# Performance work log

Hardware: AMD Instinct MI355X
Metric: run time of the kernel (lower is better)

## Reference

```python
import jax, jax.numpy as jnp
import numpy as np

N_NODES = 50000
N_EDGES = 800000
D_IN = 256
D_HID = 128
NUM_LAYERS = 6
ALPHA = 0.1
THETA = 0.5
EPS = 1e-5  # BatchNorm1d default eps


def setup_inputs() -> dict:
    key = jax.random.key(0)
    ks = jax.random.split(key, 6)
    x = jax.random.normal(ks[0], (N_NODES, D_IN), dtype=jnp.float32)
    edge_index = jax.random.randint(ks[1], (2, N_EDGES), 0, N_NODES)
    # GCNConv(D_IN, D_HID): weight + bias
    W_lin = jax.random.normal(ks[2], (D_IN, D_HID), dtype=jnp.float32) / np.sqrt(D_IN).astype(np.float32)
    b_lin = jnp.zeros((D_HID,), jnp.float32)
    # GCN2Conv weight1 per layer (shared_weights=True -> only weight1, no bias)
    W1s = jax.random.normal(ks[3], (NUM_LAYERS - 1, D_HID, D_HID), dtype=jnp.float32) / np.sqrt(D_HID).astype(np.float32)
    # BatchNorm1d affine params per intermediate layer
    bn_gamma = jnp.ones((NUM_LAYERS - 2, D_HID), jnp.float32)
    bn_beta = jnp.zeros((NUM_LAYERS - 2, D_HID), jnp.float32)
    return {"x": x, "edge_index": edge_index, "W_lin": W_lin, "b_lin": b_lin,
            "W1s": W1s, "bn_gamma": bn_gamma, "bn_beta": bn_beta}


def _gcn_conv(x, W, b, edge_index):
    # PyG GCNConv: transform, add self-loops, D^{-1/2}(A+I)D^{-1/2} aggregation.
    n = x.shape[0]
    xw = x @ W  # [N, D_HID]
    loop = jnp.arange(n)
    src = jnp.concatenate([edge_index[0], loop])
    dst = jnp.concatenate([edge_index[1], loop])
    deg = jax.ops.segment_sum(jnp.ones(src.shape, xw.dtype), dst, num_segments=n)
    dinv = jax.lax.rsqrt(jnp.maximum(deg, 1.0))  # deg >= 1 thanks to self loops
    w = dinv[src] * dinv[dst]  # [E+N]
    return jax.ops.segment_sum(xw[src] * w[:, None], dst, num_segments=n) + b


def _gcn2_conv(z, x0, W1, edge_index, beta):
    # GCN2Conv with normalize=False, shared_weights=True:
    # h = (1-alpha)*sum_{j->i} z_j + alpha*x0 ; out = (1-beta)*h + beta*(h @ W1)
    n = z.shape[0]
    agg = jax.ops.segment_sum(z[edge_index[0]], edge_index[1], num_segments=n)
    h = (1.0 - ALPHA) * agg + ALPHA * x0
    return (1.0 - beta) * h + beta * (h @ W1)


def _batchnorm(z, gamma, beta_p):
    # training-mode BatchNorm1d over the node dimension (biased variance)
    mu = jnp.mean(z, axis=0)
    var = jnp.var(z, axis=0)
    return (z - mu) * jax.lax.rsqrt(var + EPS) * gamma + beta_p


def reference(x, edge_index, W_lin, b_lin, W1s, bn_gamma, bn_beta):
    z = _gcn_conv(x, W_lin, b_lin, edge_index)
    x0 = z
    n_convs = NUM_LAYERS - 1
    # GCN2Conv layer index l = i+1 -> beta_l = log(theta/l + 1)
    betas = [float(np.log(THETA / (i + 1) + 1.0)) for i in range(n_convs)]
    for i in range(n_convs):  # dropout=0.0 -> identity, omitted
        z = _gcn2_conv(z, x0, W1s[i], edge_index, betas[i])
        if i < n_convs - 1:
            z = _batchnorm(z, bn_gamma[i], bn_beta[i])
            z = jax.nn.relu(z)
    return z
```

## Files before the change

kernel.cpp:

```cpp
#include <hip/hip_runtime.h>
#include <math.h>

#define N_NODES 50000
#define N_EDGES 800000
#define D_IN 256
#define D_HID 128
#define ALPHA 0.1f
#define EPS 1e-5f

#define NBUCK 391
#define EPB 4096
#define NBLK 196

typedef __attribute__((ext_vector_type(8))) short bf16x8;
typedef __attribute__((ext_vector_type(4))) float f32x4;

static __device__ __forceinline__ unsigned short f2bf(float f) {
    unsigned int x = __float_as_uint(f);
    return (unsigned short)((x + 0x7fffu + ((x >> 16) & 1u)) >> 16);
}
static __device__ __forceinline__ float blo(unsigned int v) {
    return __uint_as_float(v << 16);
}
static __device__ __forceinline__ float bhi(unsigned int v) {
    return __uint_as_float(v & 0xffff0000u);
}

__global__ __launch_bounds__(256) void k_hist(const int* __restrict__ dst,
                                              int* __restrict__ hist, int e) {
    __shared__ int h[NBUCK];
    int t = threadIdx.x;
    for (int i = t; i < NBUCK; i += 256) h[i] = 0;
    __syncthreads();
    int base = blockIdx.x * EPB;
    int lim = e - base;
    if (lim > EPB) lim = EPB;
    for (int i = t; i < lim; i += 256) atomicAdd(&h[dst[base + i] >> 7], 1);
    __syncthreads();
    for (int i = t; i < NBUCK; i += 256) hist[blockIdx.x * NBUCK + i] = h[i];
}

__global__ __launch_bounds__(256) void k_bkscan(const int* __restrict__ hist,
                                                int* __restrict__ offsT, int* __restrict__ btot) {
    __shared__ int sh[256];
    int b = blockIdx.x;
    int t = threadIdx.x;
    int v = (t < NBLK) ? hist[t * NBUCK + b] : 0;
    sh[t] = v;
    __syncthreads();
    for (int ofs = 1; ofs < 256; ofs <<= 1) {
        int y = (t >= ofs) ? sh[t - ofs] : 0;
        __syncthreads();
        sh[t] += y;
        __syncthreads();
    }
    if (t < NBLK) offsT[b * NBLK + t] = sh[t] - v;
    if (t == 255) btot[b] = sh[255];
}
// ... 11 lines not shown
        sh[t] += y;
        __syncthreads();
    }
    if (t < NBUCK) bbase[t] = sh[t] - v;
    if (t == 0) rp[N_NODES] = N_EDGES;
}

__global__ __launch_bounds__(256) void k_scatter(const int* __restrict__ src,
                                                 const int* __restrict__ dst,
                                                 const int* __restrict__ offsT,
                                                 const int* __restrict__ bbase,
                                                 unsigned int* __restrict__ buck, int e) {
    __shared__ int h[NBUCK];
    int t = threadIdx.x;
    for (int i = t; i < NBUCK; i += 256) h[i] = 0;
    __syncthreads();
    int base = blockIdx.x * EPB;
    int lim = e - base;
    if (lim > EPB) lim = EPB;
    for (int i = t; i < lim; i += 256) {
        int d = dst[base + i];
        int s = src[base + i];
        int b = d >> 7;
        int lp = atomicAdd(&h[b], 1);
        int pos = bbase[b] + offsT[b * NBLK + blockIdx.x] + lp;
        buck[pos] = (unsigned int)s | ((unsigned int)(d & 127) << 16);
    }
}

__global__ __launch_bounds__(256) void k_csr(const unsigned int* __restrict__ buck,
                                             const int* __restrict__ bbase,
                                             const int* __restrict__ btot,
                                             int* __restrict__ rp, float* __restrict__ dinv,
                                             int* __restrict__ cs) {
    __shared__ int dcnt[128];
    __shared__ int doff[128];
    int b = blockIdx.x;
    int t = threadIdx.x;
    if (t < 128) dcnt[t] = 0;
    __syncthreads();
    int base = bbase[b];
    int tot = btot[b];
    for (int i = t; i < tot; i += 256) {
        unsigned int v = buck[base + i];
        atomicAdd(&dcnt[(v >> 16) & 127], 1);
    }
    __syncthreads();
    if (t < 128) doff[t] = dcnt[t];
    __syncthreads();
    for (int ofs = 1; ofs < 128; ofs <<= 1) {
        int y = 0;
        if (t < 128 && t >= ofs) y = doff[t - ofs];
        __syncthreads();
        if (t < 128) doff[t] += y;
        __syncthreads();
    }
    int gd0 = b << 7;
    if (t < 128) {
        int ex = doff[t] - dcnt[t];
        if (gd0 + t < N_NODES) {
            rp[gd0 + t] = base + ex;
            dinv[gd0 + t] = rsqrtf((float)(dcnt[t] + 1));
        }
        dcnt[t] = ex;
    }
    __syncthreads();
    for (int i = t; i < tot; i += 256) {
        unsigned int v = buck[base + i];
        int p = atomicAdd(&dcnt[(v >> 16) & 127], 1);
        cs[base + p] = (int)(v & 0xffffu);
    }
}

__global__ __launch_bounds__(256) void k_cast_x(const float4* __restrict__ x, ushort2* __restrict__ xb,
                                                int n4) {
    int i = blockIdx.x * 256 + threadIdx.x;
    if (i < n4) {
        float4 v = x[i];
        ushort2 a;
        a.x = f2bf(v.x); a.y = f2bf(v.y);
        ushort2 b;
        b.x = f2bf(v.z); b.y = f2bf(v.w);
        ((ushort2*)xb)[i * 2] = a;
        ((ushort2*)xb)[i * 2 + 1] = b;
    }
}

__global__ __launch_bounds__(256) void k_prep_w(const float* __restrict__ W_lin,
                                                const float* __restrict__ W1s,
                                                unsigned short* __restrict__ Wlt,
                                                unsigned short* __restrict__ Wt) {
    int idx = blockIdx.x * 256 + threadIdx.x;
    if (idx < 128 * 256) {
        int c = idx >> 8, k = idx & 255;
        Wlt[idx] = f2bf(W_lin[k * 128 + c]);
    } else {
        int j = idx - 128 * 256;
        if (j < 5 * 128 * 128) {
            int l = j >> 14;
            int rem = j & 16383;
            int c = rem >> 7, k = rem & 127;
            float bet = logf(0.5f / (float)(l + 1) + 1.0f);
            float v = bet * W1s[l * 16384 + k * 128 + c];
            if (c == k) v += 1.0f - bet;
            Wt[j] = f2bf(v);
        }
    }
}

template <int K>
__global__ __launch_bounds__(256) void k_mgemm(const unsigned short* __restrict__ A,
                                               const unsigned short* __restrict__ Bt,
                                               unsigned short* __restrict__ outb, int M) {
    __shared__ short lds[2 * 128 * 136];
    short* As = lds;
    short* Bs = lds + 128 * 136;

    int t = threadIdx.x;
    int lane = t & 63;
    int wave = t >> 6;
    int wr = wave >> 1, wc = wave & 1;
    int row0 = blockIdx.x * 128;

    f32x4 acc[4][4];
#pragma unroll
    for (int m = 0; m < 4; ++m)
#pragma unroll
        for (int n = 0; n < 4; ++n) acc[m][n] = (f32x4){0.f, 0.f, 0.f, 0.f};

    int sr = t >> 1;
    int sh = t & 1;

    for (int k0 = 0; k0 < K; k0 += 128) {
        {
            int gr = row0 + sr;
            uint4 zero = {0, 0, 0, 0};
            const uint4* gp = (const uint4*)(A + (size_t)gr * K + k0 + sh * 64);
#pragma unroll
            for (int u = 0; u < 8; ++u) {
                uint4 v = (gr < M) ? gp[u] : zero;
                *(uint4*)(As + sr * 136 + sh * 64 + u * 8) = v;
            }
        }
        {
            const uint4* gp = (const uint4*)(Bt + (size_t)sr * K + k0 + sh * 64);
#pragma unroll
            for (int u = 0; u < 8; ++u) {
                *(uint4*)(Bs + sr * 136 + sh * 64 + u * 8) = gp[u];
            }
        }
        __syncthreads();

#pragma unroll
        for (int ks = 0; ks < 4; ++ks) {
            bf16x8 af[4], bfr[4];
#pragma unroll
            for (int m = 0; m < 4; ++m)
                af[m] = *(const bf16x8*)(As + (wr * 64 + m * 16 + (lane & 15)) * 136 + ks * 32 + (lane >> 4) * 8);
#pragma unroll
            for (int n = 0; n < 4; ++n)
                bfr[n] = *(const bf16x8*)(Bs + (wc * 64 + n * 16 + (lane & 15)) * 136 + ks * 32 + (lane >> 4) * 8);
#pragma unroll
            for (int m = 0; m < 4; ++m)
#pragma unroll
                for (int n = 0; n < 4; ++n)
                    acc[m][n] = __builtin_amdgcn_mfma_f32_16x16x32_bf16(af[m], bfr[n], acc[m][n], 0, 0, 0);
        }
        __syncthreads();
    }

    short* Z = lds;
#pragma unroll
    for (int m = 0; m < 4; ++m)
#pragma unroll
        for (int n = 0; n < 4; ++n)
#pragma unroll
            for (int r = 0; r < 4; ++r) {
                int rl = wr * 64 + m * 16 + (lane >> 4) * 4 + r;
                int cl = wc * 64 + n * 16 + (lane & 15);
                Z[rl * 136 + cl] = (short)f2bf(acc[m][n][r]);
            }
    __syncthreads();
    int gr = row0 + sr;
    if (gr < M) {
#pragma unroll
        for (int u = 0; u < 8; ++u)
            *(uint4*)(outb + (size_t)gr * 128 + sh * 64 + u * 8) = *(uint4*)(Z + sr * 136 + sh * 64 + u * 8);
    }
}

template <int MODE>
__global__ __launch_bounds__(256) void k_lgemm(const unsigned short* __restrict__ A,
                                               const unsigned short* __restrict__ Bt,
                                               unsigned short* __restrict__ outb,
                                               float* __restrict__ outf,
                                               float* __restrict__ bn_s, float* __restrict__ bn_q,
                                               int M) {
    __shared__ short As[128 * 136];
    int t = threadIdx.x;
    int lane = t & 63;
    int wave = t >> 6;
    int wr = wave >> 1, wc = wave & 1;
    int row0 = blockIdx.x * 128;

    bf16x8 bfr[4][4];
#pragma unroll
    for (int ks = 0; ks < 4; ++ks)
#pragma unroll
        for (int n = 0; n < 4; ++n)
            bfr[ks][n] = *(const bf16x8*)(Bt + (size_t)(wc * 64 + n * 16 + (lane & 15)) * 128 + ks * 32 + (lane >> 4) * 8);

    int sr = t >> 1, sh = t & 1;
    {
        int gr = row0 + sr;
// ... 60 lines not shown
        for (int m = 0; m < 4; ++m)
#pragma unroll
            for (int n = 0; n < 4; ++n)
#pragma unroll
                for (int r = 0; r < 4; ++r) {
                    int gr = row0 + wr * 64 + m * 16 + (lane >> 4) * 4 + r;
                    int cl = wc * 64 + n * 16 + (lane & 15);
                    if (gr < M) outf[(size_t)gr * 128 + cl] = acc[m][n][r];
                }
    } else {
        __syncthreads();
        short* Z = As;
#pragma unroll
        for (int m = 0; m < 4; ++m)
#pragma unroll
            for (int n = 0; n < 4; ++n)
#pragma unroll
                for (int r = 0; r < 4; ++r) {
                    int rl = wr * 64 + m * 16 + (lane >> 4) * 4 + r;
                    int cl = wc * 64 + n * 16 + (lane & 15);
                    Z[rl * 136 + cl] = (short)f2bf(acc[m][n][r]);
                }
        __syncthreads();
        int gr = row0 + sr;
        if (gr < M) {
#pragma unroll
            for (int u = 0; u < 8; ++u)
                *(uint4*)(outb + (size_t)gr * 128 + sh * 64 + u * 8) = *(uint4*)(Z + sr * 136 + sh * 64 + u * 8);
        }
    }
}

template <int MODE>
__global__ __launch_bounds__(256) void k_agg(const unsigned int* __restrict__ src,
                                             const unsigned int* __restrict__ x0b,
                                             const int* __restrict__ rp, const int* __restrict__ cs,
                                             const float* __restrict__ dinv,
                                             const float* __restrict__ b_lin,
                                             const float* __restrict__ st,
                                             unsigned int* __restrict__ dst,
                                             float* __restrict__ bns, int n) {
    if (blockIdx.x == 0) bns[threadIdx.x] = 0.f;

    int wid = (blockIdx.x * 256 + threadIdx.x) >> 6;
    int lane = threadIdx.x & 63;
    if (wid >= n) return;

    int start = __builtin_amdgcn_readfirstlane(rp[wid]);
    int end = __builtin_amdgcn_readfirstlane(rp[wid + 1]);

    float2 sc = {0.f, 0.f}, tc = {0.f, 0.f};
    if (MODE == 2) {
        sc = ((const float2*)st)[lane];
        tc = ((const float2*)st)[64 + lane];
    }
    float dn = 0.f;
    if (MODE == 0) dn = dinv[wid];

    float ax = 0.f, ay = 0.f;

    for (int base = start; base < end; base += 64) {
        int cnt = end - base;
        if (cnt > 64) cnt = 64;
        int myi = cs[base + ((lane < cnt) ? lane : 0)];
        float myw = 0.f;
        if (MODE == 0) myw = dinv[myi];

        int j = 0;
        for (; j + 7 < cnt; j += 8) {
            int s0 = __shfl(myi, j), s1 = __shfl(myi, j + 1);
            int s2 = __shfl(myi, j + 2), s3 = __shfl(myi, j + 3);
            int s4 = __shfl(myi, j + 4), s5 = __shfl(myi, j + 5);
            int s6 = __shfl(myi, j + 6), s7 = __shfl(myi, j + 7);
            unsigned int v0 = src[(size_t)s0 * 64 + lane];
            unsigned int v1 = src[(size_t)s1 * 64 + lane];
            unsigned int v2 = src[(size_t)s2 * 64 + lane];
            unsigned int v3 = src[(size_t)s3 * 64 + lane];
            unsigned int v4 = src[(size_t)s4 * 64 + lane];
            unsigned int v5 = src[(size_t)s5 * 64 + lane];
            unsigned int v6 = src[(size_t)s6 * 64 + lane];
            unsigned int v7 = src[(size_t)s7 * 64 + lane];
            if (MODE == 0) {
                float w0 = __shfl(myw, j) * dn, w1 = __shfl(myw, j + 1) * dn;
                float w2 = __shfl(myw, j + 2) * dn, w3 = __shfl(myw, j + 3) * dn;
                float w4 = __shfl(myw, j + 4) * dn, w5 = __shfl(myw, j + 5) * dn;
                float w6 = __shfl(myw, j + 6) * dn, w7 = __shfl(myw, j + 7) * dn;
                ax = fmaf(w0, blo(v0), ax); ay = fmaf(w0, bhi(v0), ay);
                ax = fmaf(w1, blo(v1), ax); ay = fmaf(w1, bhi(v1), ay);
                ax = fmaf(w2, blo(v2), ax); ay = fmaf(w2, bhi(v2), ay);
                ax = fmaf(w3, blo(v3), ax); ay = fmaf(w3, bhi(v3), ay);
                ax = fmaf(w4, blo(v4), ax); ay = fmaf(w4, bhi(v4), ay);
                ax = fmaf(w5, blo(v5), ax); ay = fmaf(w5, bhi(v5), ay);
                ax = fmaf(w6, blo(v6), ax); ay = fmaf(w6, bhi(v6), ay);
                ax = fmaf(w7, blo(v7), ax); ay = fmaf(w7, bhi(v7), ay);
            } else if (MODE == 1) {
                ax += blo(v0) + blo(v1) + blo(v2) + blo(v3) + blo(v4) + blo(v5) + blo(v6) + blo(v7);
                ay += bhi(v0) + bhi(v1) + bhi(v2) + bhi(v3) + bhi(v4) + bhi(v5) + bhi(v6) + bhi(v7);
            } else {
                ax += fmaxf(fmaf(sc.x, blo(v0), tc.x), 0.f) + fmaxf(fmaf(sc.x, blo(v1), tc.x), 0.f) +
                      fmaxf(fmaf(sc.x, blo(v2), tc.x), 0.f) + fmaxf(fmaf(sc.x, blo(v3), tc.x), 0.f) +
                      fmaxf(fmaf(sc.x, blo(v4), tc.x), 0.f) + fmaxf(fmaf(sc.x, blo(v5), tc.x), 0.f) +
                      fmaxf(fmaf(sc.x, blo(v6), tc.x), 0.f) + fmaxf(fmaf(sc.x, blo(v7), tc.x), 0.f);
                ay += fmaxf(fmaf(sc.y, bhi(v0), tc.y), 0.f) + fmaxf(fmaf(sc.y, bhi(v1), tc.y), 0.f) +
                      fmaxf(fmaf(sc.y, bhi(v2), tc.y), 0.f) + fmaxf(fmaf(sc.y, bhi(v3), tc.y), 0.f) +
                      fmaxf(fmaf(sc.y, bhi(v4), tc.y), 0.f) + fmaxf(fmaf(sc.y, bhi(v5), tc.y), 0.f) +
                      fmaxf(fmaf(sc.y, bhi(v6), tc.y), 0.f) + fmaxf(fmaf(sc.y, bhi(v7), tc.y), 0.f);
            }
        }
        for (; j < cnt; ++j) {
            int s0 = __shfl(myi, j);
            unsigned int v0 = src[(size_t)s0 * 64 + lane];
            if (MODE == 0) {
                float w0 = __shfl(myw, j) * dn;
                ax = fmaf(w0, blo(v0), ax);
                ay = fmaf(w0, bhi(v0), ay);
            } else if (MODE == 1) {
                ax += blo(v0);
                ay += bhi(v0);
            } else {
                ax += fmaxf(fmaf(sc.x, blo(v0), tc.x), 0.f);
                ay += fmaxf(fmaf(sc.y, bhi(v0), tc.y), 0.f);
            }
        }
    }

    if (MODE == 0) {
        unsigned int vs = src[(size_t)wid * 64 + lane];
        float w2 = dn * dn;
        ax = fmaf(w2, blo(vs), ax);
        ay = fmaf(w2, bhi(vs), ay);
        float2 bb = ((const float2*)b_lin)[lane];
        ax += bb.x;
        ay += bb.y;
    } else {
        unsigned int xv = x0b[(size_t)wid * 64 + lane];
        ax = fmaf(ALPHA, blo(xv), (1.0f - ALPHA) * ax);
        ay = fmaf(ALPHA, bhi(xv), (1.0f - ALPHA) * ay);
    }
    dst[(size_t)wid * 64 + lane] = (unsigned int)f2bf(ax) | ((unsigned int)f2bf(ay) << 16);
}

__global__ void k_bn_fin(const float* __restrict__ bn_s, const float* __restrict__ bn_q,
                         const float* __restrict__ gamma, const float* __restrict__ betap,
                         float* __restrict__ st, int n) {
    int c = threadIdx.x;
    float inv_n = 1.0f / (float)n;
    float mu = bn_s[c] * inv_n;
    float var = bn_q[c] * inv_n - mu * mu;
    var = fmaxf(var, 0.f);
    float s = gamma[c] * rsqrtf(var + EPS);
    st[c] = s;
    st[128 + c] = betap[c] - mu * s;
}

extern "C" void kernel_launch(void* const* d_in, const int* in_sizes, int n_in,
                              void* d_out, int out_size, void* d_ws, size_t ws_size,
                              hipStream_t stream) {
    const float* x = (const float*)d_in[0];
    const int* ei = (const int*)d_in[1];
    const float* W_lin = (const float*)d_in[2];
    const float* b_lin = (const float*)d_in[3];
    const float* W1s = (const float*)d_in[4];
    const float* gam = (const float*)d_in[5];
    const float* betp = (const float*)d_in[6];
    float* out = (float*)d_out;

    char* ws = (char*)d_ws;
    size_t off = 0;
    auto alloc = [&](size_t b) { size_t p = off; off = (off + b + 255) & ~(size_t)255; return p; };
    int* rp = (int*)(ws + alloc((size_t)(N_NODES + 1) * 4));
    int* cs = (int*)(ws + alloc((size_t)N_EDGES * 4));
    float* dinv = (float*)(ws + alloc((size_t)N_NODES * 4));
    int* hist = (int*)(ws + alloc((size_t)NBLK * NBUCK * 4));
    int* offsT = (int*)(ws + alloc((size_t)NBUCK * NBLK * 4));
    int* btot = (int*)(ws + alloc((size_t)NBUCK * 4));
    int* bbase = (int*)(ws + alloc((size_t)NBUCK * 4));
    unsigned int* buck = (unsigned int*)(ws + alloc((size_t)N_EDGES * 4));
    unsigned short* xb = (unsigned short*)(ws + alloc((size_t)N_NODES * D_IN * 2));
    unsigned short* xwb = (unsigned short*)(ws + alloc((size_t)N_NODES * D_HID * 2));
    unsigned short* x0b = (unsigned short*)(ws + alloc((size_t)N_NODES * D_HID * 2));
    unsigned short* zb = (unsigned short*)(ws + alloc((size_t)N_NODES * D_HID * 2));
    unsigned short* hb = (unsigned short*)(ws + alloc((size_t)N_NODES * D_HID * 2));
    unsigned short* Wlt = (unsigned short*)(ws + alloc((size_t)128 * 256 * 2));
    unsigned short* Wt = (unsigned short*)(ws + alloc((size_t)5 * 128 * 128 * 2));
    float* bns = (float*)(ws + alloc(256 * 4));
    float* st = (float*)(ws + alloc(256 * 4));

    const int ggrid = (N_NODES + 127) / 128;
    const int agrid = (N_NODES + 3) / 4;

    k_hist<<<NBLK, 256, 0, stream>>>(ei + N_EDGES, hist, N_EDGES);
    k_bkscan<<<NBUCK, 256, 0, stream>>>(hist, offsT, btot);
    k_bbase<<<1, 512, 0, stream>>>(btot, bbase, rp);
    k_scatter<<<NBLK, 256, 0, stream>>>(ei, ei + N_EDGES, offsT, bbase, buck, N_EDGES);
    k_csr<<<NBUCK, 256, 0, stream>>>(buck, bbase, btot, rp, dinv, cs);

    k_cast_x<<<(N_NODES * D_IN / 4 + 255) / 256, 256, 0, stream>>>((const float4*)x, (ushort2*)xb,
                                                                   N_NODES * D_IN / 4);
    k_prep_w<<<(128 * 256 + 5 * 128 * 128 + 255) / 256, 256, 0, stream>>>(W_lin, W1s, Wlt, Wt);

    k_mgemm<D_IN><<<ggrid, 256, 0, stream>>>(xb, Wlt, xwb, N_NODES);
    k_agg<0><<<agrid, 256, 0, stream>>>((const unsigned int*)xwb, nullptr, rp, cs, dinv, b_lin,
                                        nullptr, (unsigned int*)x0b, bns, N_NODES);

    for (int i = 0; i < 5; ++i) {
        const unsigned short* zsrc = (i == 0) ? x0b : zb;
        if (i == 0)
            k_agg<1><<<agrid, 256, 0, stream>>>((const unsigned int*)zsrc, (const unsigned int*)x0b,
                                                rp, cs, nullptr, nullptr, nullptr,
                                                (unsigned int*)hb, bns, N_NODES);
        else
            k_agg<2><<<agrid, 256, 0, stream>>>((const unsigned int*)zsrc, (const unsigned int*)x0b,
                                                rp, cs, nullptr, nullptr, st,
                                                (unsigned int*)hb, bns, N_NODES);
        const unsigned short* W1 = Wt + (size_t)i * 128 * 128;
        if (i < 4) {
            k_lgemm<1><<<ggrid, 256, 0, stream>>>(hb, W1, zb, nullptr, bns, bns + 128, N_NODES);
            k_bn_fin<<<1, 128, 0, stream>>>(bns, bns + 128, gam + (size_t)i * 128,
                                            betp + (size_t)i * 128, st, N_NODES);
        } else {
            k_lgemm<2><<<ggrid, 256, 0, stream>>>(hb, W1, nullptr, out, nullptr, nullptr, N_NODES);
        }
    }
}
```

Baseline: 407.7 us.

## Fuse x cast into first GEMM and vectorize aggregation with 16-byte row gathers

Removes the separate fp32-to-bf16 cast kernel for x: the first GEMM now reads fp32 rows directly and converts them while staging into shared memory, which avoids writing and re-reading the bf16 copy. The aggregation kernel now has each 16-lane quarter of a wave gather a full 256-byte row with uint4 loads, so four neighbors are processed per instruction. Partial sums are combined across quarters with xor shuffles. This trades more registers and a masked tail path for fewer, wider memory transactions per edge.

```diff
diff --git a/kernel.cpp b/kernel.cpp
--- a/kernel.cpp
+++ b/kernel.cpp
@@ -24,6 +24,12 @@
 }
 static __device__ __forceinline__ float bhi(unsigned int v) {
     return __uint_as_float(v & 0xffff0000u);
+}
+static __device__ __forceinline__ void unpack8(uint4 u, float* f) {
+    f[0] = blo(u.x); f[1] = bhi(u.x);
+    f[2] = blo(u.y); f[3] = bhi(u.y);
+    f[4] = blo(u.z); f[5] = bhi(u.z);
+    f[6] = blo(u.w); f[7] = bhi(u.w);
 }
 
 __global__ __launch_bounds__(256) void k_hist(const int* __restrict__ dst,
@@ -138,20 +144,6 @@
         unsigned int v = buck[base + i];
         int p = atomicAdd(&dcnt[(v >> 16) & 127], 1);
         cs[base + p] = (int)(v & 0xffffu);
-    }
-}
-
-__global__ __launch_bounds__(256) void k_cast_x(const float4* __restrict__ x, ushort2* __restrict__ xb,
-                                                int n4) {
-    int i = blockIdx.x * 256 + threadIdx.x;
-    if (i < n4) {
-        float4 v = x[i];
-        ushort2 a;
-        a.x = f2bf(v.x); a.y = f2bf(v.y);
-        ushort2 b;
-        b.x = f2bf(v.z); b.y = f2bf(v.w);
-        ((ushort2*)xb)[i * 2] = a;
-        ((ushort2*)xb)[i * 2 + 1] = b;
     }
 }
 
@@ -178,7 +170,7 @@
 }
 
 template <int K>
-__global__ __launch_bounds__(256) void k_mgemm(const unsigned short* __restrict__ A,
+__global__ __launch_bounds__(256) void k_mgemm(const float* __restrict__ A,
                                                const unsigned short* __restrict__ Bt,
                                                unsigned short* __restrict__ outb, int M) {
     __shared__ short lds[2 * 128 * 136];
@@ -203,12 +195,18 @@
     for (int k0 = 0; k0 < K; k0 += 128) {
         {
             int gr = row0 + sr;
-            uint4 zero = {0, 0, 0, 0};
-            const uint4* gp = (const uint4*)(A + (size_t)gr * K + k0 + sh * 64);
+            float4 zf = {0.f, 0.f, 0.f, 0.f};
+            const float4* gp = (const float4*)(A + (size_t)gr * K + k0 + sh * 64);
 #pragma unroll
             for (int u = 0; u < 8; ++u) {
-                uint4 v = (gr < M) ? gp[u] : zero;
-                *(uint4*)(As + sr * 136 + sh * 64 + u * 8) = v;
+                float4 a = (gr < M) ? gp[2 * u] : zf;
+                float4 b = (gr < M) ? gp[2 * u + 1] : zf;
+                uint4 w;
+                w.x = (unsigned int)f2bf(a.x) | ((unsigned int)f2bf(a.y) << 16);
+                w.y = (unsigned int)f2bf(a.z) | ((unsigned int)f2bf(a.w) << 16);
+                w.z = (unsigned int)f2bf(b.x) | ((unsigned int)f2bf(b.y) << 16);
+                w.w = (unsigned int)f2bf(b.z) | ((unsigned int)f2bf(b.w) << 16);
+                *(uint4*)(As + sr * 136 + sh * 64 + u * 8) = w;
             }
         }
         {
@@ -375,112 +373,165 @@
 }
 
 template <int MODE>
-__global__ __launch_bounds__(256) void k_agg(const unsigned int* __restrict__ src,
-                                             const unsigned int* __restrict__ x0b,
+__global__ __launch_bounds__(256) void k_agg(const uint4* __restrict__ src4,
+                                             const uint4* __restrict__ x04,
                                              const int* __restrict__ rp, const int* __restrict__ cs,
                                              const float* __restrict__ dinv,
                                              const float* __restrict__ b_lin,
                                              const float* __restrict__ st,
-                                             unsigned int* __restrict__ dst,
+                                             uint4* __restrict__ dst4,
                                              float* __restrict__ bns, int n) {
     if (blockIdx.x == 0) bns[threadIdx.x] = 0.f;
 
     int wid = (blockIdx.x * 256 + threadIdx.x) >> 6;
     int lane = threadIdx.x & 63;
     if (wid >= n) return;
+    int q = lane >> 4;
+    int c = lane & 15;
 
     int start = __builtin_amdgcn_readfirstlane(rp[wid]);
     int end = __builtin_amdgcn_readfirstlane(rp[wid + 1]);
 
-    float2 sc = {0.f, 0.f}, tc = {0.f, 0.f};
+    float sc[8], tc[8];
     if (MODE == 2) {
-        sc = ((const float2*)st)[lane];
-        tc = ((const float2*)st)[64 + lane];
-    }
-    float dn = 0.f;
-    if (MODE == 0) dn = dinv[wid];
-
-    float ax = 0.f, ay = 0.f;
+        float4 s0 = ((const float4*)st)[c * 2];
+        float4 s1 = ((const float4*)st)[c * 2 + 1];
+        float4 t0 = ((const float4*)st)[32 + c * 2];
+        float4 t1 = ((const float4*)st)[32 + c * 2 + 1];
+        sc[0] = s0.x; sc[1] = s0.y; sc[2] = s0.z; sc[3] = s0.w;
+        sc[4] = s1.x; sc[5] = s1.y; sc[6] = s1.z; sc[7] = s1.w;
+        tc[0] = t0.x; tc[1] = t0.y; tc[2] = t0.z; tc[3] = t0.w;
+        tc[4] = t1.x; tc[5] = t1.y; tc[6] = t1.z; tc[7] = t1.w;
+    }
+    float dn = (MODE == 0) ? dinv[wid] : 0.f;
+
+    float acc[8];
+#pragma unroll
+    for (int i = 0; i < 8; ++i) acc[i] = 0.f;
+
+#define ACCUM(vv, ww)                                                     \
+    {                                                                     \
+        float f_[8];                                                      \
+        unpack8(vv, f_);                                                  \
+        if (MODE == 0) {                                                  \
+            _Pragma("unroll") for (int i_ = 0; i_ < 8; ++i_)              \
+                acc[i_] = fmaf(ww, f_[i_], acc[i_]);                      \
+        } else if (MODE == 1) {                                           \
+            _Pragma("unroll") for (int i_ = 0; i_ < 8; ++i_)              \
+                acc[i_] += f_[i_];                                        \
+        } else {                                                          \
+            _Pragma("unroll") for (int i_ = 0; i_ < 8; ++i_)              \
+                acc[i_] += fmaxf(fmaf(sc[i_], f_[i_], tc[i_]), 0.f);      \
+        }                                                                 \
+    }
 
     for (int base = start; base < end; base += 64) {
         int cnt = end - base;
         if (cnt > 64) cnt = 64;
         int myi = cs[base + ((lane < cnt) ? lane : 0)];
-        float myw = 0.f;
-        if (MODE == 0) myw = dinv[myi];
+        float myw = (MODE == 0) ? dinv[myi] : 0.f;
 
         int j = 0;
+        for (; j + 15 < cnt; j += 16) {
+            int s0 = __shfl(myi, j + q);
+            int s1 = __shfl(myi, j + 4 + q);
+            int s2 = __shfl(myi, j + 8 + q);
+            int s3 = __shfl(myi, j + 12 + q);
+            uint4 v0 = src4[(size_t)s0 * 16 + c];
+            uint4 v1 = src4[(size_t)s1 * 16 + c];
+            uint4 v2 = src4[(size_t)s2 * 16 + c];
+            uint4 v3 = src4[(size_t)s3 * 16 + c];
+            float w0 = 0.f, w1 = 0.f, w2 = 0.f, w3 = 0.f;
+            if (MODE == 0) {
+                w0 = __shfl(myw, j + q) * dn;
+                w1 = __shfl(myw, j + 4 + q) * dn;
+                w2 = __shfl(myw, j + 8 + q) * dn;
+                w3 = __shfl(myw, j + 12 + q) * dn;
+            }
+            ACCUM(v0, w0);
+            ACCUM(v1, w1);
+            ACCUM(v2, w2);
+            ACCUM(v3, w3);
+        }
         for (; j + 7 < cnt; j += 8) {
-            int s0 = __shfl(myi, j), s1 = __shfl(myi, j + 1);
-            int s2 = __shfl(myi, j + 2), s3 = __shfl(myi, j + 3);
-            int s4 = __shfl(myi, j + 4), s5 = __shfl(myi, j + 5);
-            int s6 = __shfl(myi, j + 6), s7 = __shfl(myi, j + 7);
-            unsigned int v0 = src[(size_t)s0 * 64 + lane];
-            unsigned int v1 = src[(size_t)s1 * 64 + lane];
-            unsigned int v2 = src[(size_t)s2 * 64 + lane];
-            unsigned int v3 = src[(size_t)s3 * 64 + lane];
-            unsigned int v4 = src[(size_t)s4 * 64 + lane];
-            unsigned int v5 = src[(size_t)s5 * 64 + lane];
-            unsigned int v6 = src[(size_t)s6 * 64 + lane];
-            unsigned int v7 = src[(size_t)s7 * 64 + lane];
+            int s0 = __shfl(myi, j + q);
+            int s1 = __shfl(myi, j + 4 + q);
+            uint4 v0 = src4[(size_t)s0 * 16 + c];
+            uint4 v1 = src4[(size_t)s1 * 16 + c];
+            float w0 = 0.f, w1 = 0.f;
             if (MODE == 0) {
-                float w0 = __shfl(myw, j) * dn, w1 = __shfl(myw, j + 1) * dn;
-                float w2 = __shfl(myw, j + 2) * dn, w3 = __shfl(myw, j + 3) * dn;
-                float w4 = __shfl(myw, j + 4) * dn, w5 = __shfl(myw, j + 5) * dn;
-                float w6 = __shfl(myw, j + 6) * dn, w7 = __shfl(myw, j + 7) * dn;
-                ax = fmaf(w0, blo(v0), ax); ay = fmaf(w0, bhi(v0), ay);
-                ax = fmaf(w1, blo(v1), ax); ay = fmaf(w1, bhi(v1), ay);
-                ax = fmaf(w2, blo(v2), ax); ay = fmaf(w2, bhi(v2), ay);
-                ax = fmaf(w3, blo(v3), ax); ay = fmaf(w3, bhi(v3), ay);
-                ax = fmaf(w4, blo(v4), ax); ay = fmaf(w4, bhi(v4), ay);
-                ax = fmaf(w5, blo(v5), ax); ay = fmaf(w5, bhi(v5), ay);
-                ax = fmaf(w6, blo(v6), ax); ay = fmaf(w6, bhi(v6), ay);
-                ax = fmaf(w7, blo(v7), ax); ay = fmaf(w7, bhi(v7), ay);
-            } else if (MODE == 1) {
-                ax += blo(v0) + blo(v1) + blo(v2) + blo(v3) + blo(v4) + blo(v5) + blo(v6) + blo(v7);
-                ay += bhi(v0) + bhi(v1) + bhi(v2) + bhi(v3) + bhi(v4) + bhi(v5) + bhi(v6) + bhi(v7);
+                w0 = __shfl(myw, j + q) * dn;
+                w1 = __shfl(myw, j + 4 + q) * dn;
+            }
+            ACCUM(v0, w0);
+            ACCUM(v1, w1);
+        }
+        for (; j + 3 < cnt; j += 4) {
+            int s0 = __shfl(myi, j + q);
+            uint4 v0 = src4[(size_t)s0 * 16 + c];
+            float w0 = 0.f;
+            if (MODE == 0) w0 = __shfl(myw, j + q) * dn;
+            ACCUM(v0, w0);
+        }
+        int rem = cnt - j;
+        if (rem > 0) {
+            int jj = j + q;
+            bool act = jj < cnt;
+            int jsafe = act ? jj : (cnt - 1);
+            int s0 = __shfl(myi, jsafe);
+            uint4 v0 = src4[(size_t)s0 * 16 + c];
+            float m = act ? 1.f : 0.f;
+            if (MODE == 0) {
+                float w0 = __shfl(myw, jsafe) * dn * m;
+                ACCUM(v0, w0);
             } else {
-                ax += fmaxf(fmaf(sc.x, blo(v0), tc.x), 0.f) + fmaxf(fmaf(sc.x, blo(v1), tc.x), 0.f) +
-                      fmaxf(fmaf(sc.x, blo(v2), tc.x), 0.f) + fmaxf(fmaf(sc.x, blo(v3), tc.x), 0.f) +
-                      fmaxf(fmaf(sc.x, blo(v4), tc.x), 0.f) + fmaxf(fmaf(sc.x, blo(v5), tc.x), 0.f) +
-                      fmaxf(fmaf(sc.x, blo(v6), tc.x), 0.f) + fmaxf(fmaf(sc.x, blo(v7), tc.x), 0.f);
-                ay += fmaxf(fmaf(sc.y, bhi(v0), tc.y), 0.f) + fmaxf(fmaf(sc.y, bhi(v1), tc.y), 0.f) +
-                      fmaxf(fmaf(sc.y, bhi(v2), tc.y), 0.f) + fmaxf(fmaf(sc.y, bhi(v3), tc.y), 0.f) +
-                      fmaxf(fmaf(sc.y, bhi(v4), tc.y), 0.f) + fmaxf(fmaf(sc.y, bhi(v5), tc.y), 0.f) +
-                      fmaxf(fmaf(sc.y, bhi(v6), tc.y), 0.f) + fmaxf(fmaf(sc.y, bhi(v7), tc.y), 0.f);
+                float f_[8];
+                unpack8(v0, f_);
+                if (MODE == 1) {
+#pragma unroll
+                    for (int i_ = 0; i_ < 8; ++i_) acc[i_] = fmaf(m, f_[i_], acc[i_]);
+                } else {
+#pragma unroll
+                    for (int i_ = 0; i_ < 8; ++i_)
+                        acc[i_] = fmaf(m, fmaxf(fmaf(sc[i_], f_[i_], tc[i_]), 0.f), acc[i_]);
+                }
             }
         }
-        for (; j < cnt; ++j) {
-            int s0 = __shfl(myi, j);
-            unsigned int v0 = src[(size_t)s0 * 64 + lane];
-            if (MODE == 0) {
-                float w0 = __shfl(myw, j) * dn;
-                ax = fmaf(w0, blo(v0), ax);
-                ay = fmaf(w0, bhi(v0), ay);
-            } else if (MODE == 1) {
-                ax += blo(v0);
-                ay += bhi(v0);
-            } else {
-                ax += fmaxf(fmaf(sc.x, blo(v0), tc.x), 0.f);
-                ay += fmaxf(fmaf(sc.y, bhi(v0), tc.y), 0.f);
-            }
-        }
+    }
+#undef ACCUM
+
+#pragma unroll
+    for (int i = 0; i < 8; ++i) {
+        acc[i] += __shfl_xor(acc[i], 16);
+        acc[i] += __shfl_xor(acc[i], 32);
     }
 
     if (MODE == 0) {
-        unsigned int vs = src[(size_t)wid * 64 + lane];
+        uint4 sv = src4[(size_t)wid * 16 + c];
+        float fs[8];
+        unpack8(sv, fs);
         float w2 = dn * dn;
-        ax = fmaf(w2, blo(vs), ax);
-        ay = fmaf(w2, bhi(vs), ay);
-        float2 bb = ((const float2*)b_lin)[lane];
-        ax += bb.x;
-        ay += bb.y;
+        float4 b0 = ((const float4*)b_lin)[c * 2];
+        float4 b1 = ((const float4*)b_lin)[c * 2 + 1];
+        float bb[8] = {b0.x, b0.y, b0.z, b0.w, b1.x, b1.y, b1.z, b1.w};
+#pragma unroll
+        for (int i = 0; i < 8; ++i) acc[i] = fmaf(w2, fs[i], acc[i]) + bb[i];
     } else {
-        unsigned int xv = x0b[(size_t)wid * 64 + lane];
-        ax = fmaf(ALPHA, blo(xv), (1.0f - ALPHA) * ax);
-        ay = fmaf(ALPHA, bhi(xv), (1.0f - ALPHA) * ay);
-    }
-    dst[(size_t)wid * 64 + lane] = (unsigned int)f2bf(ax) | ((unsigned int)f2bf(ay) << 16);
+        uint4 xv = x04[(size_t)wid * 16 + c];
+        float fx[8];
+        unpack8(xv, fx);
+#pragma unroll
+        for (int i = 0; i < 8; ++i) acc[i] = fmaf(ALPHA, fx[i], (1.0f - ALPHA) * acc[i]);
+    }
+
+    if (lane < 16) {
+        uint4 o;
+        o.x = (unsigned int)f2bf(acc[0]) | ((unsigned int)f2bf(acc[1]) << 16);
+        o.y = (unsigned int)f2bf(acc[2]) | ((unsigned int)f2bf(acc[3]) << 16);
+        o.z = (unsigned int)f2bf(acc[4]) | ((unsigned int)f2bf(acc[5]) << 16);
+        o.w = (unsigned int)f2bf(acc[6]) | ((unsigned int)f2bf(acc[7]) << 16);
+        dst4[(size_t)wid * 16 + c] = o;
+    }
 }
 
 __global__ void k_bn_fin(const float* __restrict__ bn_s, const float* __restrict__ bn_q,
@@ -519,7 +570,6 @@
     int* btot = (int*)(ws + alloc((size_t)NBUCK * 4));
     int* bbase = (int*)(ws + alloc((size_t)NBUCK * 4));
     unsigned int* buck = (unsigned int*)(ws + alloc((size_t)N_EDGES * 4));
-    unsigned short* xb = (unsigned short*)(ws + alloc((size_t)N_NODES * D_IN * 2));
     unsigned short* xwb = (unsigned short*)(ws + alloc((size_t)N_NODES * D_HID * 2));
     unsigned short* x0b = (unsigned short*)(ws + alloc((size_t)N_NODES * D_HID * 2));
     unsigned short* zb = (unsigned short*)(ws + alloc((size_t)N_NODES * D_HID * 2));
@@ -538,24 +588,22 @@
     k_scatter<<<NBLK, 256, 0, stream>>>(ei, ei + N_EDGES, offsT, bbase, buck, N_EDGES);
     k_csr<<<NBUCK, 256, 0, stream>>>(buck, bbase, btot, rp, dinv, cs);
 
-    k_cast_x<<<(N_NODES * D_IN / 4 + 255) / 256, 256, 0, stream>>>((const float4*)x, (ushort2*)xb,
-                                                                   N_NODES * D_IN / 4);
     k_prep_w<<<(128 * 256 + 5 * 128 * 128 + 255) / 256, 256, 0, stream>>>(W_lin, W1s, Wlt, Wt);
 
-    k_mgemm<D_IN><<<ggrid, 256, 0, stream>>>(xb, Wlt, xwb, N_NODES);
-    k_agg<0><<<agrid, 256, 0, stream>>>((const unsigned int*)xwb, nullptr, rp, cs, dinv, b_lin,
-                                        nullptr, (unsigned int*)x0b, bns, N_NODES);
+    k_mgemm<D_IN><<<ggrid, 256, 0, stream>>>(x, Wlt, xwb, N_NODES);
+    k_agg<0><<<agrid, 256, 0, stream>>>((const uint4*)xwb, nullptr, rp, cs, dinv, b_lin,
+                                        nullptr, (uint4*)x0b, bns, N_NODES);
 
     for (int i = 0; i < 5; ++i) {
         const unsigned short* zsrc = (i == 0) ? x0b : zb;
         if (i == 0)
-            k_agg<1><<<agrid, 256, 0, stream>>>((const unsigned int*)zsrc, (const unsigned int*)x0b,
+            k_agg<1><<<agrid, 256, 0, stream>>>((const uint4*)zsrc, (const uint4*)x0b,
                                                 rp, cs, nullptr, nullptr, nullptr,
-                                                (unsigned int*)hb, bns, N_NODES);
+                                                (uint4*)hb, bns, N_NODES);
         else
-            k_agg<2><<<agrid, 256, 0, stream>>>((const unsigned int*)zsrc, (const unsigned int*)x0b,
+            k_agg<2><<<agrid, 256, 0, stream>>>((const uint4*)zsrc, (const uint4*)x0b,
                                                 rp, cs, nullptr, nullptr, st,
-                                                (unsigned int*)hb, bns, N_NODES);
+                                                (uint4*)hb, bns, N_NODES);
         const unsigned short* W1 = Wt + (size_t)i * 128 * 128;
         if (i < 4) {
             k_lgemm<1><<<ggrid, 256, 0, stream>>>(hb, W1, zb, nullptr, bns, bns + 128, N_NODES);
```

New measurement: 432.5 us. 6.1% more time.

## Split aggregation per node across column slices with edge-parallel rows

Applied to the files above, without the earlier changes.

The neighbor-aggregation kernel now gives each node to 8 blocks, one per 16-feature column slice. Within a wave, 8 lanes groups handle different edges in parallel and the partial sums are combined with xor-shuffles before one group writes the result. Column indices are also stored as 16-bit values to halve index traffic. The aim is fewer serial gather steps per node and more memory-level parallelism, at the cost of 8x more blocks, repeated index and row-pointer reads per node, and narrower 32-byte gathers per neighbor row.

```diff
diff --git a/kernel.cpp b/kernel.cpp
--- a/kernel.cpp
+++ b/kernel.cpp
@@ -101,7 +101,7 @@
                                              const int* __restrict__ bbase,
                                              const int* __restrict__ btot,
                                              int* __restrict__ rp, float* __restrict__ dinv,
-                                             int* __restrict__ cs) {
+                                             unsigned short* __restrict__ cs) {
     __shared__ int dcnt[128];
     __shared__ int doff[128];
     int b = blockIdx.x;
@@ -137,7 +137,7 @@
     for (int i = t; i < tot; i += 256) {
         unsigned int v = buck[base + i];
         int p = atomicAdd(&dcnt[(v >> 16) & 127], 1);
-        cs[base + p] = (int)(v & 0xffffu);
+        cs[base + p] = (unsigned short)(v & 0xffffu);
     }
 }
 
@@ -150,8 +150,8 @@
         a.x = f2bf(v.x); a.y = f2bf(v.y);
         ushort2 b;
         b.x = f2bf(v.z); b.y = f2bf(v.w);
-        ((ushort2*)xb)[i * 2] = a;
-        ((ushort2*)xb)[i * 2 + 1] = b;
+        xb[i * 2] = a;
+        xb[i * 2 + 1] = b;
     }
 }
 
@@ -375,9 +375,10 @@
 }
 
 template <int MODE>
-__global__ __launch_bounds__(256) void k_agg(const unsigned int* __restrict__ src,
-                                             const unsigned int* __restrict__ x0b,
-                                             const int* __restrict__ rp, const int* __restrict__ cs,
+__global__ __launch_bounds__(256) void k_agg(const unsigned int* __restrict__ zsrc,
+                                             const unsigned int* __restrict__ x0,
+                                             const int* __restrict__ rp,
+                                             const unsigned short* __restrict__ cs,
                                              const float* __restrict__ dinv,
                                              const float* __restrict__ b_lin,
                                              const float* __restrict__ st,
@@ -385,102 +386,108 @@
                                              float* __restrict__ bns, int n) {
     if (blockIdx.x == 0) bns[threadIdx.x] = 0.f;
 
-    int wid = (blockIdx.x * 256 + threadIdx.x) >> 6;
+    int slice = blockIdx.x & 7;
+    int wid = (blockIdx.x >> 3) * 4 + (threadIdx.x >> 6);
     int lane = threadIdx.x & 63;
     if (wid >= n) return;
+    int r = lane >> 3;
+    int c = lane & 7;
+    int sofs = slice * 8 + c;
 
     int start = __builtin_amdgcn_readfirstlane(rp[wid]);
     int end = __builtin_amdgcn_readfirstlane(rp[wid + 1]);
 
-    float2 sc = {0.f, 0.f}, tc = {0.f, 0.f};
+    float sc0 = 0.f, sc1 = 0.f, tc0 = 0.f, tc1 = 0.f;
     if (MODE == 2) {
-        sc = ((const float2*)st)[lane];
-        tc = ((const float2*)st)[64 + lane];
-    }
-    float dn = 0.f;
-    if (MODE == 0) dn = dinv[wid];
-
-    float ax = 0.f, ay = 0.f;
+        float2 s = ((const float2*)st)[slice * 8 + c];
+        float2 tt = ((const float2*)st)[64 + slice * 8 + c];
+        sc0 = s.x; sc1 = s.y; tc0 = tt.x; tc1 = tt.y;
+    }
+    float dn = (MODE == 0) ? dinv[wid] : 0.f;
+    float a0 = 0.f, a1 = 0.f;
 
     for (int base = start; base < end; base += 64) {
         int cnt = end - base;
         if (cnt > 64) cnt = 64;
-        int myi = cs[base + ((lane < cnt) ? lane : 0)];
-        float myw = 0.f;
-        if (MODE == 0) myw = dinv[myi];
-
-        int j = 0;
-        for (; j + 7 < cnt; j += 8) {
-            int s0 = __shfl(myi, j), s1 = __shfl(myi, j + 1);
-            int s2 = __shfl(myi, j + 2), s3 = __shfl(myi, j + 3);
-            int s4 = __shfl(myi, j + 4), s5 = __shfl(myi, j + 5);
-            int s6 = __shfl(myi, j + 6), s7 = __shfl(myi, j + 7);
-            unsigned int v0 = src[(size_t)s0 * 64 + lane];
-            unsigned int v1 = src[(size_t)s1 * 64 + lane];
-            unsigned int v2 = src[(size_t)s2 * 64 + lane];
-            unsigned int v3 = src[(size_t)s3 * 64 + lane];
-            unsigned int v4 = src[(size_t)s4 * 64 + lane];
-            unsigned int v5 = src[(size_t)s5 * 64 + lane];
-            unsigned int v6 = src[(size_t)s6 * 64 + lane];
-            unsigned int v7 = src[(size_t)s7 * 64 + lane];
+        int li = (lane < cnt) ? lane : (cnt - 1);
+        int myi = (int)cs[base + li];
+        float myw = (MODE == 0) ? dinv[myi] : 0.f;
+
+        int ng = cnt >> 3;
+        int g = 0;
+        for (; g + 1 < ng; g += 2) {
+            int j0 = g * 8 + r, j1 = j0 + 8;
+            int i0 = __shfl(myi, j0);
+            int i1 = __shfl(myi, j1);
+            unsigned int v0 = zsrc[(size_t)i0 * 64 + sofs];
+            unsigned int v1 = zsrc[(size_t)i1 * 64 + sofs];
             if (MODE == 0) {
-                float w0 = __shfl(myw, j) * dn, w1 = __shfl(myw, j + 1) * dn;
-                float w2 = __shfl(myw, j + 2) * dn, w3 = __shfl(myw, j + 3) * dn;
-                float w4 = __shfl(myw, j + 4) * dn, w5 = __shfl(myw, j + 5) * dn;
-                float w6 = __shfl(myw, j + 6) * dn, w7 = __shfl(myw, j + 7) * dn;
-                ax = fmaf(w0, blo(v0), ax); ay = fmaf(w0, bhi(v0), ay);
-                ax = fmaf(w1, blo(v1), ax); ay = fmaf(w1, bhi(v1), ay);
-                ax = fmaf(w2, blo(v2), ax); ay = fmaf(w2, bhi(v2), ay);
-                ax = fmaf(w3, blo(v3), ax); ay = fmaf(w3, bhi(v3), ay);
-                ax = fmaf(w4, blo(v4), ax); ay = fmaf(w4, bhi(v4), ay);
-                ax = fmaf(w5, blo(v5), ax); ay = fmaf(w5, bhi(v5), ay);
-                ax = fmaf(w6, blo(v6), ax); ay = fmaf(w6, bhi(v6), ay);
-                ax = fmaf(w7, blo(v7), ax); ay = fmaf(w7, bhi(v7), ay);
+                float w0 = __shfl(myw, j0) * dn;
+                float w1 = __shfl(myw, j1) * dn;
+                a0 = fmaf(w0, blo(v0), a0); a1 = fmaf(w0, bhi(v0), a1);
+                a0 = fmaf(w1, blo(v1), a0); a1 = fmaf(w1, bhi(v1), a1);
             } else if (MODE == 1) {
-                ax += blo(v0) + blo(v1) + blo(v2) + blo(v3) + blo(v4) + blo(v5) + blo(v6) + blo(v7);
-                ay += bhi(v0) + bhi(v1) + bhi(v2) + bhi(v3) + bhi(v4) + bhi(v5) + bhi(v6) + bhi(v7);
+                a0 += blo(v0) + blo(v1);
+                a1 += bhi(v0) + bhi(v1);
             } else {
-                ax += fmaxf(fmaf(sc.x, blo(v0), tc.x), 0.f) + fmaxf(fmaf(sc.x, blo(v1), tc.x), 0.f) +
-                      fmaxf(fmaf(sc.x, blo(v2), tc.x), 0.f) + fmaxf(fmaf(sc.x, blo(v3), tc.x), 0.f) +
-                      fmaxf(fmaf(sc.x, blo(v4), tc.x), 0.f) + fmaxf(fmaf(sc.x, blo(v5), tc.x), 0.f) +
-                      fmaxf(fmaf(sc.x, blo(v6), tc.x), 0.f) + fmaxf(fmaf(sc.x, blo(v7), tc.x), 0.f);
-                ay += fmaxf(fmaf(sc.y, bhi(v0), tc.y), 0.f) + fmaxf(fmaf(sc.y, bhi(v1), tc.y), 0.f) +
-                      fmaxf(fmaf(sc.y, bhi(v2), tc.y), 0.f) + fmaxf(fmaf(sc.y, bhi(v3), tc.y), 0.f) +
-                      fmaxf(fmaf(sc.y, bhi(v4), tc.y), 0.f) + fmaxf(fmaf(sc.y, bhi(v5), tc.y), 0.f) +
-                      fmaxf(fmaf(sc.y, bhi(v6), tc.y), 0.f) + fmaxf(fmaf(sc.y, bhi(v7), tc.y), 0.f);
-            }
-        }
-        for (; j < cnt; ++j) {
-            int s0 = __shfl(myi, j);
-            unsigned int v0 = src[(size_t)s0 * 64 + lane];
+                a0 += fmaxf(fmaf(sc0, blo(v0), tc0), 0.f) + fmaxf(fmaf(sc0, blo(v1), tc0), 0.f);
+                a1 += fmaxf(fmaf(sc1, bhi(v0), tc1), 0.f) + fmaxf(fmaf(sc1, bhi(v1), tc1), 0.f);
+            }
+        }
+        for (; g < ng; ++g) {
+            int j0 = g * 8 + r;
+            int i0 = __shfl(myi, j0);
+            unsigned int v0 = zsrc[(size_t)i0 * 64 + sofs];
             if (MODE == 0) {
-                float w0 = __shfl(myw, j) * dn;
-                ax = fmaf(w0, blo(v0), ax);
-                ay = fmaf(w0, bhi(v0), ay);
+                float w0 = __shfl(myw, j0) * dn;
+                a0 = fmaf(w0, blo(v0), a0); a1 = fmaf(w0, bhi(v0), a1);
             } else if (MODE == 1) {
-                ax += blo(v0);
-                ay += bhi(v0);
+                a0 += blo(v0);
+                a1 += bhi(v0);
             } else {
-                ax += fmaxf(fmaf(sc.x, blo(v0), tc.x), 0.f);
-                ay += fmaxf(fmaf(sc.y, bhi(v0), tc.y), 0.f);
-            }
-        }
-    }
-
-    if (MODE == 0) {
-        unsigned int vs = src[(size_t)wid * 64 + lane];
-        float w2 = dn * dn;
-        ax = fmaf(w2, blo(vs), ax);
-        ay = fmaf(w2, bhi(vs), ay);
-        float2 bb = ((const float2*)b_lin)[lane];
-        ax += bb.x;
-        ay += bb.y;
-    } else {
-        unsigned int xv = x0b[(size_t)wid * 64 + lane];
-        ax = fmaf(ALPHA, blo(xv), (1.0f - ALPHA) * ax);
-        ay = fmaf(ALPHA, bhi(xv), (1.0f - ALPHA) * ay);
-    }
-    dst[(size_t)wid * 64 + lane] = (unsigned int)f2bf(ax) | ((unsigned int)f2bf(ay) << 16);
+                a0 += fmaxf(fmaf(sc0, blo(v0), tc0), 0.f);
+                a1 += fmaxf(fmaf(sc1, bhi(v0), tc1), 0.f);
+            }
+        }
+        int rem = cnt & 7;
+        if (rem) {
+            int j = ng * 8 + r;
+            bool act = r < rem;
+            int js = act ? j : (cnt - 1);
+            int i0 = __shfl(myi, js);
+            unsigned int v0 = zsrc[(size_t)i0 * 64 + sofs];
+            float m = act ? 1.f : 0.f;
+            if (MODE == 0) {
+                float w0 = __shfl(myw, js) * dn * m;
+                a0 = fmaf(w0, blo(v0), a0); a1 = fmaf(w0, bhi(v0), a1);
+            } else if (MODE == 1) {
+                a0 = fmaf(m, blo(v0), a0);
+                a1 = fmaf(m, bhi(v0), a1);
+            } else {
+                a0 = fmaf(m, fmaxf(fmaf(sc0, blo(v0), tc0), 0.f), a0);
+                a1 = fmaf(m, fmaxf(fmaf(sc1, bhi(v0), tc1), 0.f), a1);
+            }
+        }
+    }
+
+    a0 += __shfl_xor(a0, 8);  a1 += __shfl_xor(a1, 8);
+    a0 += __shfl_xor(a0, 16); a1 += __shfl_xor(a1, 16);
+    a0 += __shfl_xor(a0, 32); a1 += __shfl_xor(a1, 32);
+
+    if (lane < 8) {
+        if (MODE == 0) {
+            unsigned int vs = zsrc[(size_t)wid * 64 + sofs];
+            float w2 = dn * dn;
+            float2 bb = ((const float2*)b_lin)[slice * 8 + c];
+            a0 = fmaf(w2, blo(vs), a0) + bb.x;
+            a1 = fmaf(w2, bhi(vs), a1) + bb.y;
+        } else {
+            unsigned int xv = x0[(size_t)wid * 64 + sofs];
+            a0 = fmaf(ALPHA, blo(xv), (1.0f - ALPHA) * a0);
+            a1 = fmaf(ALPHA, bhi(xv), (1.0f - ALPHA) * a1);
+        }
+        dst[(size_t)wid * 64 + sofs] = (unsigned int)f2bf(a0) | ((unsigned int)f2bf(a1) << 16);
+    }
 }
 
 __global__ void k_bn_fin(const float* __restrict__ bn_s, const float* __restrict__ bn_q,
@@ -512,7 +519,7 @@
     size_t off = 0;
     auto alloc = [&](size_t b) { size_t p = off; off = (off + b + 255) & ~(size_t)255; return p; };
     int* rp = (int*)(ws + alloc((size_t)(N_NODES + 1) * 4));
-    int* cs = (int*)(ws + alloc((size_t)N_EDGES * 4));
+    unsigned short* cs = (unsigned short*)(ws + alloc((size_t)N_EDGES * 2));
     float* dinv = (float*)(ws + alloc((size_t)N_NODES * 4));
     int* hist = (int*)(ws + alloc((size_t)NBLK * NBUCK * 4));
     int* offsT = (int*)(ws + alloc((size_t)NBUCK * NBLK * 4));
@@ -530,7 +537,7 @@
     float* st = (float*)(ws + alloc(256 * 4));
 
     const int ggrid = (N_NODES + 127) / 128;
-    const int agrid = (N_NODES + 3) / 4;
+    const int agrid = ((N_NODES + 3) / 4) * 8;
 
     k_hist<<<NBLK, 256, 0, stream>>>(ei + N_EDGES, hist, N_EDGES);
     k_bkscan<<<NBUCK, 256, 0, stream>>>(hist, offsT, btot);
```

New measurement: 956.0 us. 135% more time.

## Fold source-side degree scaling into first GEMM and shrink CSR column indices to 16-bit

Applied to the files above, without the earlier changes.

The first GEMM epilogue now scales each output row by dinv, so the first aggregation becomes a plain sum followed by one multiply by the destination's dinv. This removes the per-edge dinv gather and the weight shuffles. Column indices are stored as unsigned short, which halves index traffic in every aggregation pass. The 16-bit indices cannot represent node ids above 65535; they are safe here only because N_NODES is 50000. The row scaling also applies bf16 rounding after the dinv multiply, which slightly changes numerics.

```diff
diff --git a/kernel.cpp b/kernel.cpp
--- a/kernel.cpp
+++ b/kernel.cpp
@@ -101,7 +101,7 @@
                                              const int* __restrict__ bbase,
                                              const int* __restrict__ btot,
                                              int* __restrict__ rp, float* __restrict__ dinv,
-                                             int* __restrict__ cs) {
+                                             unsigned short* __restrict__ cs) {
     __shared__ int dcnt[128];
     __shared__ int doff[128];
     int b = blockIdx.x;
@@ -137,7 +137,7 @@
     for (int i = t; i < tot; i += 256) {
         unsigned int v = buck[base + i];
         int p = atomicAdd(&dcnt[(v >> 16) & 127], 1);
-        cs[base + p] = (int)(v & 0xffffu);
+        cs[base + p] = (unsigned short)(v & 0xffffu);
     }
 }
 
@@ -150,8 +150,8 @@
         a.x = f2bf(v.x); a.y = f2bf(v.y);
         ushort2 b;
         b.x = f2bf(v.z); b.y = f2bf(v.w);
-        ((ushort2*)xb)[i * 2] = a;
-        ((ushort2*)xb)[i * 2 + 1] = b;
+        xb[i * 2] = a;
+        xb[i * 2 + 1] = b;
     }
 }
 
@@ -180,6 +180,7 @@
 template <int K>
 __global__ __launch_bounds__(256) void k_mgemm(const unsigned short* __restrict__ A,
                                                const unsigned short* __restrict__ Bt,
+                                               const float* __restrict__ dinv,
                                                unsigned short* __restrict__ outb, int M) {
     __shared__ short lds[2 * 128 * 136];
     short* As = lds;
@@ -242,13 +243,16 @@
 #pragma unroll
     for (int m = 0; m < 4; ++m)
 #pragma unroll
-        for (int n = 0; n < 4; ++n)
-#pragma unroll
-            for (int r = 0; r < 4; ++r) {
-                int rl = wr * 64 + m * 16 + (lane >> 4) * 4 + r;
+        for (int r = 0; r < 4; ++r) {
+            int rl = wr * 64 + m * 16 + (lane >> 4) * 4 + r;
+            int grow = row0 + rl;
+            float dv = (grow < M) ? dinv[grow] : 0.f;
+#pragma unroll
+            for (int n = 0; n < 4; ++n) {
                 int cl = wc * 64 + n * 16 + (lane & 15);
-                Z[rl * 136 + cl] = (short)f2bf(acc[m][n][r]);
+                Z[rl * 136 + cl] = (short)f2bf(acc[m][n][r] * dv);
             }
+        }
     __syncthreads();
     int gr = row0 + sr;
     if (gr < M) {
@@ -377,7 +381,8 @@
 template <int MODE>
 __global__ __launch_bounds__(256) void k_agg(const unsigned int* __restrict__ src,
                                              const unsigned int* __restrict__ x0b,
-                                             const int* __restrict__ rp, const int* __restrict__ cs,
+                                             const int* __restrict__ rp,
+                                             const unsigned short* __restrict__ cs,
                                              const float* __restrict__ dinv,
                                              const float* __restrict__ b_lin,
                                              const float* __restrict__ st,
@@ -397,17 +402,13 @@
         sc = ((const float2*)st)[lane];
         tc = ((const float2*)st)[64 + lane];
     }
-    float dn = 0.f;
-    if (MODE == 0) dn = dinv[wid];
 
     float ax = 0.f, ay = 0.f;
 
     for (int base = start; base < end; base += 64) {
         int cnt = end - base;
         if (cnt > 64) cnt = 64;
-        int myi = cs[base + ((lane < cnt) ? lane : 0)];
-        float myw = 0.f;
-        if (MODE == 0) myw = dinv[myi];
+        int myi = (int)cs[base + ((lane < cnt) ? lane : (cnt - 1))];
 
         int j = 0;
         for (; j + 7 < cnt; j += 8) {
@@ -423,23 +424,7 @@
             unsigned int v5 = src[(size_t)s5 * 64 + lane];
             unsigned int v6 = src[(size_t)s6 * 64 + lane];
             unsigned int v7 = src[(size_t)s7 * 64 + lane];
-            if (MODE == 0) {
-                float w0 = __shfl(myw, j) * dn, w1 = __shfl(myw, j + 1) * dn;
-                float w2 = __shfl(myw, j + 2) * dn, w3 = __shfl(myw, j + 3) * dn;
-                float w4 = __shfl(myw, j + 4) * dn, w5 = __shfl(myw, j + 5) * dn;
-                float w6 = __shfl(myw, j + 6) * dn, w7 = __shfl(myw, j + 7) * dn;
-                ax = fmaf(w0, blo(v0), ax); ay = fmaf(w0, bhi(v0), ay);
-                ax = fmaf(w1, blo(v1), ax); ay = fmaf(w1, bhi(v1), ay);
-                ax = fmaf(w2, blo(v2), ax); ay = fmaf(w2, bhi(v2), ay);
-                ax = fmaf(w3, blo(v3), ax); ay = fmaf(w3, bhi(v3), ay);
-                ax = fmaf(w4, blo(v4), ax); ay = fmaf(w4, bhi(v4), ay);
-                ax = fmaf(w5, blo(v5), ax); ay = fmaf(w5, bhi(v5), ay);
-                ax = fmaf(w6, blo(v6), ax); ay = fmaf(w6, bhi(v6), ay);
-                ax = fmaf(w7, blo(v7), ax); ay = fmaf(w7, bhi(v7), ay);
-            } else if (MODE == 1) {
-                ax += blo(v0) + blo(v1) + blo(v2) + blo(v3) + blo(v4) + blo(v5) + blo(v6) + blo(v7);
-                ay += bhi(v0) + bhi(v1) + bhi(v2) + bhi(v3) + bhi(v4) + bhi(v5) + bhi(v6) + bhi(v7);
-            } else {
+            if (MODE == 2) {
                 ax += fmaxf(fmaf(sc.x, blo(v0), tc.x), 0.f) + fmaxf(fmaf(sc.x, blo(v1), tc.x), 0.f) +
                       fmaxf(fmaf(sc.x, blo(v2), tc.x), 0.f) + fmaxf(fmaf(sc.x, blo(v3), tc.x), 0.f) +
                       fmaxf(fmaf(sc.x, blo(v4), tc.x), 0.f) + fmaxf(fmaf(sc.x, blo(v5), tc.x), 0.f) +
@@ -448,33 +433,30 @@
                       fmaxf(fmaf(sc.y, bhi(v2), tc.y), 0.f) + fmaxf(fmaf(sc.y, bhi(v3), tc.y), 0.f) +
                       fmaxf(fmaf(sc.y, bhi(v4), tc.y), 0.f) + fmaxf(fmaf(sc.y, bhi(v5), tc.y), 0.f) +
                       fmaxf(fmaf(sc.y, bhi(v6), tc.y), 0.f) + fmaxf(fmaf(sc.y, bhi(v7), tc.y), 0.f);
+            } else {
+                ax += blo(v0) + blo(v1) + blo(v2) + blo(v3) + blo(v4) + blo(v5) + blo(v6) + blo(v7);
+                ay += bhi(v0) + bhi(v1) + bhi(v2) + bhi(v3) + bhi(v4) + bhi(v5) + bhi(v6) + bhi(v7);
             }
         }
         for (; j < cnt; ++j) {
             int s0 = __shfl(myi, j);
             unsigned int v0 = src[(size_t)s0 * 64 + lane];
-            if (MODE == 0) {
-                float w0 = __shfl(myw, j) * dn;
-                ax = fmaf(w0, blo(v0), ax);
-                ay = fmaf(w0, bhi(v0), ay);
-            } else if (MODE == 1) {
+            if (MODE == 2) {
+                ax += fmaxf(fmaf(sc.x, blo(v0), tc.x), 0.f);
+                ay += fmaxf(fmaf(sc.y, bhi(v0), tc.y), 0.f);
+            } else {
                 ax += blo(v0);
                 ay += bhi(v0);
-            } else {
-                ax += fmaxf(fmaf(sc.x, blo(v0), tc.x), 0.f);
-                ay += fmaxf(fmaf(sc.y, bhi(v0), tc.y), 0.f);
             }
         }
     }
 
     if (MODE == 0) {
         unsigned int vs = src[(size_t)wid * 64 + lane];
-        float w2 = dn * dn;
-        ax = fmaf(w2, blo(vs), ax);
-        ay = fmaf(w2, bhi(vs), ay);
+        float dn = dinv[wid];
         float2 bb = ((const float2*)b_lin)[lane];
-        ax += bb.x;
-        ay += bb.y;
+        ax = (ax + blo(vs)) * dn + bb.x;
+        ay = (ay + bhi(vs)) * dn + bb.y;
     } else {
         unsigned int xv = x0b[(size_t)wid * 64 + lane];
         ax = fmaf(ALPHA, blo(xv), (1.0f - ALPHA) * ax);
@@ -512,7 +494,7 @@
     size_t off = 0;
     auto alloc = [&](size_t b) { size_t p = off; off = (off + b + 255) & ~(size_t)255; return p; };
     int* rp = (int*)(ws + alloc((size_t)(N_NODES + 1) * 4));
-    int* cs = (int*)(ws + alloc((size_t)N_EDGES * 4));
+    unsigned short* cs = (unsigned short*)(ws + alloc((size_t)N_EDGES * 2));
     float* dinv = (float*)(ws + alloc((size_t)N_NODES * 4));
     int* hist = (int*)(ws + alloc((size_t)NBLK * NBUCK * 4));
     int* offsT = (int*)(ws + alloc((size_t)NBUCK * NBLK * 4));
@@ -542,7 +524,7 @@
                                                                    N_NODES * D_IN / 4);
     k_prep_w<<<(128 * 256 + 5 * 128 * 128 + 255) / 256, 256, 0, stream>>>(W_lin, W1s, Wlt, Wt);
 
-    k_mgemm<D_IN><<<ggrid, 256, 0, stream>>>(xb, Wlt, xwb, N_NODES);
+    k_mgemm<D_IN><<<ggrid, 256, 0, stream>>>(xb, Wlt, dinv, xwb, N_NODES);
     k_agg<0><<<agrid, 256, 0, stream>>>((const unsigned int*)xwb, nullptr, rp, cs, dinv, b_lin,
                                         nullptr, (unsigned int*)x0b, bns, N_NODES);
 
```

Measured after the change: 400.6 us. About the same (-1.7%).
